# Optimization experiments

Measured on AMD Instinct MI355X. Metric: run time of the kernel, lower is better.

The kernel has to match this reference:

```python
import jax, jax.numpy as jnp
import numpy as np
import math

B, S, HID = 128, 200, 1024
NH = 4
DK = HID // NH
LSESS = 200  # session_len
MAXSEQ = 200
EPS = 1e-12


def setup_inputs() -> dict:
    key = jax.random.key(0)
    ks = jax.random.split(key, 12)
    inp = {}
    inp['query'] = jax.random.normal(ks[0], (B, S, HID), jnp.float32)
    inp['key'] = jax.random.normal(ks[1], (B, S, HID), jnp.float32)
    inp['value'] = jax.random.normal(ks[2], (B, S, HID), jnp.float32)
    std = 0.05
    inp['attn_w0'] = std * jax.random.normal(ks[3], (DK, DK), jnp.float32)
    inp['attn_w1'] = std * jax.random.normal(ks[4], (DK, DK), jnp.float32)
    inp['attn_w2'] = std * jax.random.normal(ks[5], (DK, DK), jnp.float32)
    inp['attn_w3'] = std * jax.random.normal(ks[6], (LSESS, DK), jnp.float32)
    inp['attn_bias'] = jnp.zeros((DK,), jnp.float32)
    inp['complex_weight'] = 0.02 * jax.random.normal(ks[7], (1, NH, MAXSEQ // 2 + 1, DK, 2), jnp.float32)
    bound = 1.0 / math.sqrt(HID)
    inp['linear_w'] = jax.random.uniform(ks[8], (HID, HID), jnp.float32, -bound, bound)
    inp['linear_b'] = jax.random.uniform(ks[9], (HID,), jnp.float32, -bound, bound)
    inp['ln_w'] = jnp.ones((HID,), jnp.float32)
    inp['ln_b'] = jnp.zeros((HID,), jnp.float32)
    return inp


def _gelu(x):
    return x * 0.5 * (1.0 + jax.lax.erf(x / jnp.sqrt(jnp.asarray(2.0, x.dtype))))


def reference(query, key, value, attn_w0, attn_w1, attn_w2, attn_w3, attn_bias,
              complex_weight, linear_w, linear_b, ln_w, ln_b):
    nb = query.shape[0]
    # (B, S, H, DK) -> (B, H, S, DK)
    def split_heads(x):
        return x.reshape(nb, -1, NH, DK).transpose(0, 2, 1, 3)
    q, k, v = split_heads(query), split_heads(key), split_heads(value)

    q = q @ attn_w0
    k = k @ attn_w1
    v = v @ attn_w2

    qf = jnp.fft.rfft(q, axis=2, norm='ortho')   # (B,H,S//2+1,DK) complex
    kf = jnp.fft.rfft(k, axis=2, norm='ortho')
    weight = complex_weight[..., 0] + 1j * complex_weight[..., 1]  # (1,4,MAXSEQ//2+1,DK)
    res = qf * jnp.conj(kf) * weight
    corr = jnp.fft.irfft(res, n=MAXSEQ, axis=2, norm='ortho')       # (B,H,MAXSEQ,DK)

    alpha = jnp.matmul(jax.nn.relu(corr + attn_bias), attn_w3.T)    # (B,H,MAXSEQ,LSESS)
    alpha = jax.nn.softmax(alpha, axis=-2)                          # softmax over seq dim
    x = jnp.einsum('bhsl,bhsd->bhld', alpha, v)                     # (B,H,LSESS,DK)

    x = x.transpose(0, 2, 1, 3).reshape(nb, -1, NH * DK)            # (B,LSESS,HID)
    x = x @ linear_w.T + linear_b
    # dropout is identity at inference
    x = _gelu(x)
    # LayerNorm (TF-style, eps inside sqrt)
    u = x.mean(-1, keepdims=True)
    s = ((x - u) ** 2).mean(-1, keepdims=True)
    x = (x - u) / jnp.sqrt(s + EPS)
    return ln_w * x + ln_b
```

## Files before the change

### kernel.cpp

```cpp
#include <hip/hip_runtime.h>
#include <hip/hip_bf16.h>
#include <math.h>

#define BATCH 128
#define SEQ   200
#define HID   1024
#define NH    4
#define DK    256
#define NF    101
#define NF2   202
#define LS    200
#define PD    256

typedef __attribute__((ext_vector_type(8))) short bf16x8;
typedef __attribute__((ext_vector_type(4))) float f32x4;

__device__ __forceinline__ unsigned short f2bf(float f) {
    union { float f; unsigned u; } v; v.f = f;
    unsigned r = v.u + 0x7fff + ((v.u >> 16) & 1);
    return (unsigned short)(r >> 16);
}
__device__ __forceinline__ float bf2f(unsigned short h) {
    union { unsigned u; float f; } v; v.u = ((unsigned)h) << 16;
    return v.f;
}

__device__ __forceinline__ void gld_lds16(const void* g, void* l) {
    __builtin_amdgcn_global_load_lds(
        (const __attribute__((address_space(1))) unsigned*)g,
        (__attribute__((address_space(3))) unsigned*)l, 16, 0, 0);
}

#define KSWZ(row, c8) ((c8) ^ (((row) & 7) << 3))

__global__ void init_tables_bf16(unsigned short* __restrict__ F, unsigned short* __restrict__ G) {
    int idx = blockIdx.x * 256 + threadIdx.x;
    const double inv = 0.07071067811865475244;
    const double PI2 = 6.283185307179586476925;
    {
        int fidx = idx >> 8, s = idx & 255;
        double v = 0.0;
        if (s < SEQ && fidx < NF2) {
            int f = (fidx < NF) ? fidx : fidx - NF;
            double ang = PI2 * (double)((f * s) % SEQ) / (double)SEQ;
            v = (fidx < NF) ? cos(ang) * inv : -sin(ang) * inv;
        }
        F[idx] = f2bf((float)v);
    }
    {
        int s = idx >> 8, j = idx & 255;
        double v = 0.0;
        if (s < SEQ && j < NF2) {
            if (j < NF) {
                double al = (j == 0 || j == NF - 1) ? 1.0 : 2.0;
                v = al * cos(PI2 * (double)((j * s) % SEQ) / (double)SEQ) * inv;
            } else {
                int f = j - NF;
                if (f != 0 && f != NF - 1)
                    v = -2.0 * sin(PI2 * (double)((f * s) % SEQ) / (double)SEQ) * inv;
            }
        }
        G[idx] = f2bf((float)v);
    }
}

__global__ void wtrans256(const float* __restrict__ src, unsigned short* __restrict__ dst) {
    int dout = blockIdx.x, din = threadIdx.x;
    dst[dout * 256 + din] = f2bf(src[din * 256 + dout]);
}

__global__ void w3pad(const float* __restrict__ src, unsigned short* __restrict__ dst) {
    int row = blockIdx.x, col = threadIdx.x;
    dst[row * 256 + col] = (row < LS) ? f2bf(src[row * 256 + col]) : (unsigned short)0;
}

__global__ void fconv(const float* __restrict__ src, unsigned short* __restrict__ dst, int n) {
    int i = blockIdx.x * 256 + threadIdx.x;
    if (i < n) dst[i] = f2bf(src[i]);
}

__global__ __launch_bounds__(256)
void mgemm128(const unsigned short* __restrict__ A, const float* __restrict__ Bf0,
              unsigned short* __restrict__ C0,
              int K, int lda, int ldb, int ldc,
              long aOuter, long aInner, long bOuter, long bInner,
              long cOuter, long cInner, int nInner, int nbValid) {
    int bz = blockIdx.z;
    int bo = bz / nInner, bi = bz - bo * nInner;
    const unsigned short* Ab = A + bo * aOuter + bi * aInner;
    const float* Bf = Bf0 + bo * bOuter + bi * bInner;

    __shared__ unsigned short As[128 * 64];
    __shared__ unsigned short Bs[128 * 64];

    int t = threadIdx.x;
    int m0 = blockIdx.y * 128, n0 = blockIdx.x * 128;
    int lane = t & 63, wave = t >> 6;
    int wr = wave >> 1, wc = wave & 1;
    int la = lane & 15, hi = lane >> 4;

    f32x4 acc[4][4] = {};
    int rsub = t >> 3;
    int c8 = (t & 7) * 8;

    for (int k0 = 0; k0 < K; k0 += 64) {
#pragma unroll
        for (int p = 0; p < 4; ++p) {
            int row = p * 32 + rsub;
            gld_lds16(Ab + (long)(m0 + row) * lda + k0 + KSWZ(row, c8), &As[row * 64 + c8]);
        }
#pragma unroll
        for (int p = 0; p < 4; ++p) {
            int row = p * 32 + rsub;
            int gn = n0 + row;
            unsigned short tmp[8];
            if (gn < nbValid) {
                const float4* src = reinterpret_cast<const float4*>(Bf + (long)gn * ldb + k0 + c8);
                float4 x0 = src[0], x1 = src[1];
                tmp[0] = f2bf(x0.x); tmp[1] = f2bf(x0.y); tmp[2] = f2bf(x0.z); tmp[3] = f2bf(x0.w);
                tmp[4] = f2bf(x1.x); tmp[5] = f2bf(x1.y); tmp[6] = f2bf(x1.z); tmp[7] = f2bf(x1.w);
            } else {
#pragma unroll
                for (int j = 0; j < 8; ++j) tmp[j] = 0;
            }
            *(bf16x8*)&Bs[row * 64 + KSWZ(row, c8)] = *(bf16x8*)tmp;
        }
        __syncthreads();
#pragma unroll
        for (int half = 0; half < 2; ++half) {
            int ko = half * 32 + hi * 8;
            bf16x8 a[4], b[4];
#pragma unroll
            for (int mi = 0; mi < 4; ++mi) {
                int ra = wr * 64 + mi * 16 + la;
                a[mi] = *(const bf16x8*)&As[ra * 64 + KSWZ(ra, ko)];
            }
#pragma unroll
            for (int ni = 0; ni < 4; ++ni) {
                int rb = wc * 64 + ni * 16 + la;
                b[ni] = *(const bf16x8*)&Bs[rb * 64 + KSWZ(rb, ko)];
            }
#pragma unroll
            for (int mi = 0; mi < 4; ++mi)
#pragma unroll
                for (int ni = 0; ni < 4; ++ni)
                    acc[mi][ni] = __builtin_amdgcn_mfma_f32_16x16x32_bf16(a[mi], b[ni], acc[mi][ni], 0, 0, 0);
        }
        __syncthreads();
    }

    unsigned short* Ch = C0 + bo * cOuter + bi * cInner;
#pragma unroll
    for (int mi = 0; mi < 4; ++mi) {
#pragma unroll
        for (int ni = 0; ni < 4; ++ni) {
            int gn = n0 + wc * 64 + ni * 16 + la;
            int gmB = m0 + wr * 64 + mi * 16 + hi * 4;
#pragma unroll
            for (int rr = 0; rr < 4; ++rr)
                Ch[(long)(gmB + rr) * ldc + gn] = f2bf(acc[mi][ni][rr]);
        }
    }
}

template <int EPI, bool XCDSWZ>
__global__ __launch_bounds__(512, 2)
void mgemm256(const unsigned short* __restrict__ A, const unsigned short* __restrict__ B,
              unsigned short* __restrict__ C0, int K, int lda, int ldb, int ldc,
              long aOuter, long aInner, long bOuter, long bInner,
              long cOuter, long cInner, int nInner, int mValid,
              const float* __restrict__ biasN) {
    extern __shared__ unsigned short lds[];
    unsigned short* AsB = lds;
    unsigned short* BsB = lds + 32768;

    int bx = blockIdx.x, by = blockIdx.y;
    if (XCDSWZ) {
        int nwg = gridDim.x * gridDim.y;
        int flat = by * gridDim.x + bx;
        int cpx = nwg >> 3;
        int swz = (flat & 7) * cpx + (flat >> 3);
        bx = swz % gridDim.x; by = swz / gridDim.x;
    }
    int bz = blockIdx.z;
    int bo = bz / nInner, bi = bz - bo * nInner;
    const unsigned short* Ab = A + bo * aOuter + bi * aInner;
    const unsigned short* Bb = B + bo * bOuter + bi * bInner;

    int t = threadIdx.x;
    int m0 = by * 256, n0 = bx * 256;
    int lane = t & 63, wave = t >> 6;
    int wr = wave >> 2, wc = wave & 3;
    int la = lane & 15, hi = lane >> 4;

    f32x4 acc[8][4] = {};
    int rsub = t >> 3;
    int c8 = (t & 7) * 8;

    auto stageA = [&](unsigned short* dst, long k0, int h) {
#pragma unroll
        for (int p = 0; p < 2; ++p) {
            int row = h * 128 + p * 64 + rsub;
            gld_lds16(Ab + (long)(m0 + row) * lda + k0 + KSWZ(row, c8), &dst[row * 64 + c8]);
        }
    };
    auto stageB = [&](unsigned short* dst, long k0, int h) {
#pragma unroll
        for (int p = 0; p < 2; ++p) {
            int row = h * 128 + p * 64 + rsub;
            gld_lds16(Bb + (long)(n0 + row) * ldb + k0 + KSWZ(row, c8), &dst[row * 64 + c8]);
        }
    };
    auto ldf = [&](const unsigned short* P, int row, int ko) -> bf16x8 {
        return *(const bf16x8*)&P[row * 64 + KSWZ(row, ko)];
    };

#define MFMA_ROW(mi, xa) \
    acc[mi][0] = __builtin_amdgcn_mfma_f32_16x16x32_bf16(xa, b0, acc[mi][0], 0, 0, 0); \
    acc[mi][1] = __builtin_amdgcn_mfma_f32_16x16x32_bf16(xa, b1, acc[mi][1], 0, 0, 0); \
    acc[mi][2] = __builtin_amdgcn_mfma_f32_16x16x32_bf16(xa, b2, acc[mi][2], 0, 0, 0); \
    acc[mi][3] = __builtin_amdgcn_mfma_f32_16x16x32_bf16(xa, b3, acc[mi][3], 0, 0, 0);

    int nkt = K >> 6;
    stageA(AsB, 0, 0); stageA(AsB, 0, 1);
    stageB(BsB, 0, 0); stageB(BsB, 0, 1);

    for (int kt = 0; kt < nkt; ++kt) {
        int cur = kt & 1;
        const unsigned short* Ac = AsB + cur * 16384;
        const unsigned short* Bc = BsB + cur * 16384;
        unsigned short* An = AsB + (cur ^ 1) * 16384;
        unsigned short* Bn = BsB + (cur ^ 1) * 16384;
        bool pre = (kt + 1) < nkt;
        long kn = (long)(kt + 1) << 6;

        bf16x8 b0, b1, b2, b3;

        if (pre) {
            stageA(An, kn, 0);
            asm volatile("s_waitcnt vmcnt(2)" ::: "memory");
        } else {
            asm volatile("s_waitcnt vmcnt(0)" ::: "memory");
        }
        __builtin_amdgcn_s_barrier();
        __builtin_amdgcn_sched_barrier(0);
        {
            int ko = hi * 8;
            b0 = ldf(Bc, wc * 64 + 0 * 16 + la, ko);
            b1 = ldf(Bc, wc * 64 + 1 * 16 + la, ko);
            b2 = ldf(Bc, wc * 64 + 2 * 16 + la, ko);
            b3 = ldf(Bc, wc * 64 + 3 * 16 + la, ko);
            bf16x8 x0 = ldf(Ac, wr * 128 + 0 * 16 + la, ko);
            bf16x8 x1 = ldf(Ac, wr * 128 + 1 * 16 + la, ko);
            bf16x8 x2 = ldf(Ac, wr * 128 + 2 * 16 + la, ko);
            bf16x8 x3 = ldf(Ac, wr * 128 + 3 * 16 + la, ko);
            __builtin_amdgcn_s_setprio(1);
            MFMA_ROW(0, x0) MFMA_ROW(1, x1) MFMA_ROW(2, x2) MFMA_ROW(3, x3)
            __builtin_amdgcn_s_setprio(0);
        }
        __builtin_amdgcn_s_barrier();

        if (pre) stageA(An, kn, 1);
        {
            int ko = hi * 8;
            bf16x8 x4 = ldf(Ac, wr * 128 + 4 * 16 + la, ko);
            bf16x8 x5 = ldf(Ac, wr * 128 + 5 * 16 + la, ko);
            bf16x8 x6 = ldf(Ac, wr * 128 + 6 * 16 + la, ko);
            bf16x8 x7 = ldf(Ac, wr * 128 + 7 * 16 + la, ko);
            __builtin_amdgcn_s_setprio(1);
            MFMA_ROW(4, x4) MFMA_ROW(5, x5) MFMA_ROW(6, x6) MFMA_ROW(7, x7)
            __builtin_amdgcn_s_setprio(0);
        }
        __builtin_amdgcn_s_barrier();

        if (pre) stageB(Bn, kn, 0);
        {
            int ko = 32 + hi * 8;
            b0 = ldf(Bc, wc * 64 + 0 * 16 + la, ko);
            b1 = ldf(Bc, wc * 64 + 1 * 16 + la, ko);
            b2 = ldf(Bc, wc * 64 + 2 * 16 + la, ko);
            b3 = ldf(Bc, wc * 64 + 3 * 16 + la, ko);
            bf16x8 x0 = ldf(Ac, wr * 128 + 0 * 16 + la, ko);
            bf16x8 x1 = ldf(Ac, wr * 128 + 1 * 16 + la, ko);
            bf16x8 x2 = ldf(Ac, wr * 128 + 2 * 16 + la, ko);
            bf16x8 x3 = ldf(Ac, wr * 128 + 3 * 16 + la, ko);
            __builtin_amdgcn_s_setprio(1);
            MFMA_ROW(0, x0) MFMA_ROW(1, x1) MFMA_ROW(2, x2) MFMA_ROW(3, x3)
            __builtin_amdgcn_s_setprio(0);
        }
        __builtin_amdgcn_s_barrier();

        if (pre) stageB(Bn, kn, 1);
        {
            int ko = 32 + hi * 8;
            bf16x8 x4 = ldf(Ac, wr * 128 + 4 * 16 + la, ko);
            bf16x8 x5 = ldf(Ac, wr * 128 + 5 * 16 + la, ko);
            bf16x8 x6 = ldf(Ac, wr * 128 + 6 * 16 + la, ko);
            bf16x8 x7 = ldf(Ac, wr * 128 + 7 * 16 + la, ko);
            __builtin_amdgcn_s_setprio(1);
            MFMA_ROW(4, x4) MFMA_ROW(5, x5) MFMA_ROW(6, x6) MFMA_ROW(7, x7)
            __builtin_amdgcn_s_setprio(0);
        }
        __builtin_amdgcn_s_barrier();
    }
#undef MFMA_ROW

    unsigned short* Ch = C0 + bo * cOuter + bi * cInner;
#pragma unroll
    for (int mi = 0; mi < 8; ++mi) {
#pragma unroll
        for (int ni = 0; ni < 4; ++ni) {
            int gn = n0 + wc * 64 + ni * 16 + la;
            int gmB = m0 + wr * 128 + mi * 16 + hi * 4;
            float bN = 0.f;
            if (EPI == 2 || EPI == 4) bN = biasN[gn];
#pragma unroll
            for (int rr = 0; rr < 4; ++rr) {
                int gm = gmB + rr;
                if (gm >= mValid) continue;
                float v = acc[mi][ni][rr];
                if (EPI == 0) Ch[(long)gm * ldc + gn] = f2bf(v);
                else if (EPI == 2) Ch[(long)gm * ldc + gn] = f2bf(fmaxf(v + bN, 0.f));
                else Ch[(long)gm * ldc + gn] = f2bf(v + bN);
            }
        }
    }
}

__global__ void crossspec(unsigned short* __restrict__ QF, const unsigned short* __restrict__ KF,
                          const float* __restrict__ cw) {
    long idx = (long)blockIdx.x * 256 + threadIdx.x;
    if (idx >= (long)BATCH * NH * DK * NF) return;
    int f = (int)(idx % NF);
    long tq = idx / NF;
    int d = (int)(tq % DK);
    int bh = (int)(tq / DK);
    int h = bh & (NH - 1);
    long base = (long)bh * DK * PD + (long)d * PD;
    float qr = bf2f(QF[base + f]), qi = bf2f(QF[base + NF + f]);
    float kr = bf2f(KF[base + f]), ki = bf2f(KF[base + NF + f]);
    float cr = qr * kr + qi * ki;
    float ci = qi * kr - qr * ki;
    long wb = (((long)h * NF + f) * DK + d) * 2;
    float wr = cw[wb], wi = cw[wb + 1];
    QF[base + f]      = f2bf(cr * wr - ci * wi);
    QF[base + NF + f] = f2bf(cr * wi + ci * wr);
    if (f < PD - NF2) QF[base + NF2 + f] = 0;
}

__global__ __launch_bounds__(256) void softmax_rows(const unsigned short* __restrict__ in,
                                                    unsigned short* __restrict__ out) {
    long row = (long)blockIdx.x * 4 + (threadIdx.x >> 6);
    int lane = threadIdx.x & 63;
    const unsigned short* p = in + row * PD;
    float v[4];
    float m = -1e30f;
#pragma unroll
    for (int i = 0; i < 4; ++i) {
        int s = lane + 64 * i;
        v[i] = (s < SEQ) ? bf2f(p[s]) : -1e30f;
        m = fmaxf(m, v[i]);
    }
#pragma unroll
    for (int o = 32; o; o >>= 1) m = fmaxf(m, __shfl_xor(m, o));
    float e[4], sum = 0.f;
#pragma unroll
    for (int i = 0; i < 4; ++i) {
        int s = lane + 64 * i;
        e[i] = (s < SEQ) ? expf(v[i] - m) : 0.f;
        sum += e[i];
    }
#pragma unroll
    for (int o = 32; o; o >>= 1) sum += __shfl_xor(sum, o);
    float inv = 1.f / sum;
    unsigned short* q = out + row * PD;
#pragma unroll
    for (int i = 0; i < 4; ++i) {
        int s = lane + 64 * i;
        q[s] = (s < SEQ) ? f2bf(e[i] * inv) : (unsigned short)0;
    }
}

__global__ __launch_bounds__(256) void gelu_ln_kernel(const unsigned short* __restrict__ y2,
                               const float* __restrict__ lnw, const float* __restrict__ lnb,
                               float* __restrict__ out) {
    long row = blockIdx.x;
    int tid = threadIdx.x;
    const short4* xr = reinterpret_cast<const short4*>(y2 + row * HID);
    short4 h4 = xr[tid];
    float g[4];
    {
        float x0 = bf2f((unsigned short)h4.x), x1 = bf2f((unsigned short)h4.y);
        float x2 = bf2f((unsigned short)h4.z), x3 = bf2f((unsigned short)h4.w);
        g[0] = 0.5f * x0 * (1.f + erff(x0 * 0.70710678118654752f));
        g[1] = 0.5f * x1 * (1.f + erff(x1 * 0.70710678118654752f));
        g[2] = 0.5f * x2 * (1.f + erff(x2 * 0.70710678118654752f));
        g[3] = 0.5f * x3 * (1.f + erff(x3 * 0.70710678118654752f));
    }

    __shared__ float red[4];
    float s = g[0] + g[1] + g[2] + g[3];
#pragma unroll
    for (int o = 32; o > 0; o >>= 1) s += __shfl_down(s, o);
    if ((tid & 63) == 0) red[tid >> 6] = s;
    __syncthreads();
    float mean = (red[0] + red[1] + red[2] + red[3]) * (1.f / (float)HID);

    float v2 = 0.f;
#pragma unroll
    for (int p = 0; p < 4; ++p) { float d = g[p] - mean; v2 += d * d; }
    __syncthreads();
#pragma unroll
    for (int o = 32; o > 0; o >>= 1) v2 += __shfl_down(v2, o);
    if ((tid & 63) == 0) red[tid >> 6] = v2;
    __syncthreads();
    float var = (red[0] + red[1] + red[2] + red[3]) * (1.f / (float)HID);
    float rstd = rsqrtf(var + 1e-12f);

    float4 o4;
    int i0 = tid * 4;
    o4.x = (g[0] - mean) * rstd * lnw[i0 + 0] + lnb[i0 + 0];
    o4.y = (g[1] - mean) * rstd * lnw[i0 + 1] + lnb[i0 + 1];
    o4.z = (g[2] - mean) * rstd * lnw[i0 + 2] + lnb[i0 + 2];
    o4.w = (g[3] - mean) * rstd * lnw[i0 + 3] + lnb[i0 + 3];
    reinterpret_cast<float4*>(out + row * HID)[tid] = o4;
}

extern "C" void kernel_launch(void* const* d_in, const int* in_sizes, int n_in,
                              void* d_out, int out_size, void* d_ws, size_t ws_size,
                              hipStream_t stream) {
    const float* query = (const float*)d_in[0];
    const float* key   = (const float*)d_in[1];
    const float* value = (const float*)d_in[2];
    const float* w0 = (const float*)d_in[3];
    const float* w1 = (const float*)d_in[4];
    const float* w2 = (const float*)d_in[5];
    const float* w3 = (const float*)d_in[6];
    const float* attn_bias = (const float*)d_in[7];
    const float* cw = (const float*)d_in[8];
    const float* lw = (const float*)d_in[9];
    const float* lb = (const float*)d_in[10];
    const float* lnw = (const float*)d_in[11];
    const float* lnb = (const float*)d_in[12];
    float* out = (float*)d_out;

    char* base = (char*)d_ws;
    const long BH = (long)BATCH * NH;
    const long SZR = (long)BH * PD * PD;
    const size_t M64 = 67108864;

    unsigned short* F_stack = (unsigned short*)(base + 0);
    unsigned short* G_stack = (unsigned short*)(base + 131072);
    unsigned short* w0T = (unsigned short*)(base + 262144);
    unsigned short* w1T = (unsigned short*)(base + 393216);
    unsigned short* w2T = (unsigned short*)(base + 524288);
    unsigned short* w3b = (unsigned short*)(base + 655360);
    unsigned short* lwb = (unsigned short*)(base + 786432);
    char* rA = base + 4194304;
    char* rB = rA + M64;
    char* rC = rB + M64;
    char* rD = rC + M64;
    char* rE = rD + M64;

    unsigned short* qpT = (unsigned short*)rA;
    unsigned short* kpT = (unsigned short*)rB;
    unsigned short* vpT = (unsigned short*)rC;
    unsigned short* QF  = (unsigned short*)rD;
    unsigned short* KF  = (unsigned short*)rE;
    unsigned short* corr = (unsigned short*)rA;
    unsigned short* alphaT = (unsigned short*)rD;
    unsigned short* probs = (unsigned short*)rB;
    unsigned short* X  = (unsigned short*)rE;
    unsigned short* y2 = (unsigned short*)rD;

    const size_t LDS256 = 131072;

    init_tables_bf16<<<256, 256, 0, stream>>>(F_stack, G_stack);
    wtrans256<<<256, 256, 0, stream>>>(w0, w0T);
    wtrans256<<<256, 256, 0, stream>>>(w1, w1T);
    wtrans256<<<256, 256, 0, stream>>>(w2, w2T);
    w3pad<<<256, 256, 0, stream>>>(w3, w3b);
    fconv<<<(HID * HID + 255) / 256, 256, 0, stream>>>(lw, lwb, HID * HID);

    dim3 gproj(2, 2, BH);
    mgemm128<<<gproj, 256, 0, stream>>>(w0T, query, qpT, DK, DK, HID, PD,
        0L, 0L, (long)SEQ * HID, (long)DK, (long)NH * PD * PD, (long)PD * PD, NH, SEQ);
    mgemm128<<<gproj, 256, 0, stream>>>(w1T, key, kpT, DK, DK, HID, PD,
        0L, 0L, (long)SEQ * HID, (long)DK, (long)NH * PD * PD, (long)PD * PD, NH, SEQ);
    mgemm128<<<gproj, 256, 0, stream>>>(w2T, value, vpT, DK, DK, HID, PD,
        0L, 0L, (long)SEQ * HID, (long)DK, (long)NH * PD * PD, (long)PD * PD, NH, SEQ);

    mgemm256<0, false><<<dim3(1, 1, 2 * BH), 512, LDS256, stream>>>(
        qpT, F_stack, QF, PD, PD, PD, PD,
        SZR, (long)PD * PD, 0L, 0L, SZR, (long)PD * PD, (int)BH, PD, nullptr);

    long ncs = (long)BH * DK * NF;
    crossspec<<<(unsigned)((ncs + 255) / 256), 256, 0, stream>>>(QF, KF, cw);

    mgemm256<2, false><<<dim3(1, 1, BH), 512, LDS256, stream>>>(
        G_stack, QF, corr, PD, PD, PD, PD,
        0L, 0L, (long)PD * PD, 0L, (long)PD * PD, 0L, 1, PD, attn_bias);

    mgemm256<0, false><<<dim3(1, 1, BH), 512, LDS256, stream>>>(
        w3b, corr, alphaT, PD, PD, PD, PD,
        0L, 0L, (long)PD * PD, 0L, (long)PD * PD, 0L, 1, PD, nullptr);

    softmax_rows<<<(unsigned)(BH * PD / 4), 256, 0, stream>>>(alphaT, probs);

    mgemm256<0, false><<<dim3(1, 1, BH), 512, LDS256, stream>>>(
        probs, vpT, X, PD, PD, PD, HID,
        (long)NH * PD * PD, (long)PD * PD,
        (long)NH * PD * PD, (long)PD * PD,
        (long)LS * HID, (long)DK, NH, LS, nullptr);

    mgemm256<4, true><<<dim3(HID / 256, (BATCH * LS) / 256, 1), 512, LDS256, stream>>>(
        X, lwb, y2, HID, HID, HID, HID,
        0L, 0L, 0L, 0L, 0L, 0L, 1, BATCH * LS, lb);

    gelu_ln_kernel<<<(unsigned)(BATCH * LS), 256, 0, stream>>>(y2, lnw, lnb, out);
}
```

Baseline: 605.1 us.

## Fuse alpha GEMM with softmax, merge QKV projections, vectorize cross-spectrum

The three QKV projection GEMMs are merged into one launch with 256x256 tiles, one block per (tensor, batch, head). The alpha GEMM and the separate softmax kernel become one kernel that does the softmax in registers using shuffles plus LDS reductions, so the alpha matrix never makes a round trip through global memory. The DFT tables now put the imaginary part at offset 128, which lets crossspec use aligned 8-wide vector loads with one block per batch-head. In exchange there is more register and LDS pressure in the fused kernel, and the projection kernel's B-operand staging is still synchronous.

```diff
diff --git a/kernel.cpp b/kernel.cpp
--- a/kernel.cpp
+++ b/kernel.cpp
@@ -8,9 +8,9 @@
 #define NH    4
 #define DK    256
 #define NF    101
-#define NF2   202
 #define LS    200
 #define PD    256
+#define IMOFF 128
 
 typedef __attribute__((ext_vector_type(8))) short bf16x8;
 typedef __attribute__((ext_vector_type(4))) float f32x4;
@@ -40,22 +40,25 @@
     {
         int fidx = idx >> 8, s = idx & 255;
         double v = 0.0;
-        if (s < SEQ && fidx < NF2) {
-            int f = (fidx < NF) ? fidx : fidx - NF;
-            double ang = PI2 * (double)((f * s) % SEQ) / (double)SEQ;
-            v = (fidx < NF) ? cos(ang) * inv : -sin(ang) * inv;
+        if (s < SEQ) {
+            if (fidx < NF) {
+                v = cos(PI2 * (double)((fidx * s) % SEQ) / (double)SEQ) * inv;
+            } else if (fidx >= IMOFF && fidx < IMOFF + NF) {
+                int f = fidx - IMOFF;
+                v = -sin(PI2 * (double)((f * s) % SEQ) / (double)SEQ) * inv;
+            }
         }
         F[idx] = f2bf((float)v);
     }
     {
         int s = idx >> 8, j = idx & 255;
         double v = 0.0;
-        if (s < SEQ && j < NF2) {
+        if (s < SEQ) {
             if (j < NF) {
                 double al = (j == 0 || j == NF - 1) ? 1.0 : 2.0;
                 v = al * cos(PI2 * (double)((j * s) % SEQ) / (double)SEQ) * inv;
-            } else {
-                int f = j - NF;
+            } else if (j >= IMOFF && j < IMOFF + NF) {
+                int f = j - IMOFF;
                 if (f != 0 && f != NF - 1)
                     v = -2.0 * sin(PI2 * (double)((f * s) % SEQ) / (double)SEQ) * inv;
             }
@@ -79,44 +82,43 @@
     if (i < n) dst[i] = f2bf(src[i]);
 }
 
-__global__ __launch_bounds__(256)
-void mgemm128(const unsigned short* __restrict__ A, const float* __restrict__ Bf0,
-              unsigned short* __restrict__ C0,
-              int K, int lda, int ldb, int ldc,
-              long aOuter, long aInner, long bOuter, long bInner,
-              long cOuter, long cInner, int nInner, int nbValid) {
-    int bz = blockIdx.z;
-    int bo = bz / nInner, bi = bz - bo * nInner;
-    const unsigned short* Ab = A + bo * aOuter + bi * aInner;
-    const float* Bf = Bf0 + bo * bOuter + bi * bInner;
-
-    __shared__ unsigned short As[128 * 64];
-    __shared__ unsigned short Bs[128 * 64];
+__global__ __launch_bounds__(512, 2)
+void mgemm256f(const unsigned short* __restrict__ Wall,
+               const float* __restrict__ Q, const float* __restrict__ Kt,
+               const float* __restrict__ V, unsigned short* __restrict__ C0) {
+    __shared__ unsigned short As[256 * 64];
+    __shared__ unsigned short Bs[256 * 64];
+
+    int bz = blockIdx.x;
+    int sel = bz >> 9;
+    int bh = bz & 511;
+    int b = bh >> 2, h = bh & 3;
+    const unsigned short* A = Wall + sel * 65536;
+    const float* Bf = ((sel == 0) ? Q : (sel == 1) ? Kt : V) + (long)b * SEQ * HID + h * DK;
+    unsigned short* Ch = C0 + (long)sel * 33554432 + (long)bh * PD * PD;
 
     int t = threadIdx.x;
-    int m0 = blockIdx.y * 128, n0 = blockIdx.x * 128;
     int lane = t & 63, wave = t >> 6;
-    int wr = wave >> 1, wc = wave & 1;
+    int wr = wave >> 2, wc = wave & 3;
     int la = lane & 15, hi = lane >> 4;
-
-    f32x4 acc[4][4] = {};
     int rsub = t >> 3;
     int c8 = (t & 7) * 8;
 
-    for (int k0 = 0; k0 < K; k0 += 64) {
+    f32x4 acc[8][4] = {};
+
+    for (int k0 = 0; k0 < 256; k0 += 64) {
 #pragma unroll
         for (int p = 0; p < 4; ++p) {
-            int row = p * 32 + rsub;
-            gld_lds16(Ab + (long)(m0 + row) * lda + k0 + KSWZ(row, c8), &As[row * 64 + c8]);
+            int row = p * 64 + rsub;
+            gld_lds16(A + (long)row * 256 + k0 + KSWZ(row, c8), &As[row * 64 + c8]);
         }
 #pragma unroll
         for (int p = 0; p < 4; ++p) {
-            int row = p * 32 + rsub;
-            int gn = n0 + row;
+            int row = p * 64 + rsub;
             unsigned short tmp[8];
-            if (gn < nbValid) {
-                const float4* src = reinterpret_cast<const float4*>(Bf + (long)gn * ldb + k0 + c8);
-                float4 x0 = src[0], x1 = src[1];
+            if (row < SEQ) {
+                const float4* s4 = reinterpret_cast<const float4*>(Bf + (long)row * HID + k0 + c8);
+                float4 x0 = s4[0], x1 = s4[1];
                 tmp[0] = f2bf(x0.x); tmp[1] = f2bf(x0.y); tmp[2] = f2bf(x0.z); tmp[3] = f2bf(x0.w);
                 tmp[4] = f2bf(x1.x); tmp[5] = f2bf(x1.y); tmp[6] = f2bf(x1.z); tmp[7] = f2bf(x1.w);
             } else {
@@ -129,36 +131,37 @@
 #pragma unroll
         for (int half = 0; half < 2; ++half) {
             int ko = half * 32 + hi * 8;
-            bf16x8 a[4], b[4];
-#pragma unroll
-            for (int mi = 0; mi < 4; ++mi) {
-                int ra = wr * 64 + mi * 16 + la;
-                a[mi] = *(const bf16x8*)&As[ra * 64 + KSWZ(ra, ko)];
-            }
+            bf16x8 bb[4], xx[8];
 #pragma unroll
             for (int ni = 0; ni < 4; ++ni) {
                 int rb = wc * 64 + ni * 16 + la;
-                b[ni] = *(const bf16x8*)&Bs[rb * 64 + KSWZ(rb, ko)];
-            }
-#pragma unroll
-            for (int mi = 0; mi < 4; ++mi)
+                bb[ni] = *(const bf16x8*)&Bs[rb * 64 + KSWZ(rb, ko)];
+            }
+#pragma unroll
+            for (int mi = 0; mi < 8; ++mi) {
+                int ra = wr * 128 + mi * 16 + la;
+                xx[mi] = *(const bf16x8*)&As[ra * 64 + KSWZ(ra, ko)];
+            }
+            __builtin_amdgcn_s_setprio(1);
+#pragma unroll
+            for (int mi = 0; mi < 8; ++mi)
 #pragma unroll
                 for (int ni = 0; ni < 4; ++ni)
-                    acc[mi][ni] = __builtin_amdgcn_mfma_f32_16x16x32_bf16(a[mi], b[ni], acc[mi][ni], 0, 0, 0);
+                    acc[mi][ni] = __builtin_amdgcn_mfma_f32_16x16x32_bf16(xx[mi], bb[ni], acc[mi][ni], 0, 0, 0);
+            __builtin_amdgcn_s_setprio(0);
         }
         __syncthreads();
     }
 
-    unsigned short* Ch = C0 + bo * cOuter + bi * cInner;
-#pragma unroll
-    for (int mi = 0; mi < 4; ++mi) {
+#pragma unroll
+    for (int mi = 0; mi < 8; ++mi) {
 #pragma unroll
         for (int ni = 0; ni < 4; ++ni) {
-            int gn = n0 + wc * 64 + ni * 16 + la;
-            int gmB = m0 + wr * 64 + mi * 16 + hi * 4;
+            int gn = wc * 64 + ni * 16 + la;
+            int gmB = wr * 128 + mi * 16 + hi * 4;
 #pragma unroll
             for (int rr = 0; rr < 4; ++rr)
-                Ch[(long)(gmB + rr) * ldc + gn] = f2bf(acc[mi][ni][rr]);
+                Ch[(long)(gmB + rr) * PD + gn] = f2bf(acc[mi][ni][rr]);
         }
     }
 }
@@ -327,57 +330,225 @@
     }
 }
 
-__global__ void crossspec(unsigned short* __restrict__ QF, const unsigned short* __restrict__ KF,
-                          const float* __restrict__ cw) {
-    long idx = (long)blockIdx.x * 256 + threadIdx.x;
-    if (idx >= (long)BATCH * NH * DK * NF) return;
-    int f = (int)(idx % NF);
-    long tq = idx / NF;
-    int d = (int)(tq % DK);
-    int bh = (int)(tq / DK);
+__global__ __launch_bounds__(512, 2)
+void alphasm(const unsigned short* __restrict__ A, const unsigned short* __restrict__ B,
+             unsigned short* __restrict__ P0) {
+    extern __shared__ unsigned short lds[];
+    unsigned short* AsB = lds;
+    unsigned short* BsB = lds + 32768;
+    __shared__ float redM[256][4];
+    __shared__ float redS[256][4];
+
+    int bh = blockIdx.x;
+    const unsigned short* Ab = A;
+    const unsigned short* Bb = B + (long)bh * PD * PD;
+
+    int t = threadIdx.x;
+    int lane = t & 63, wave = t >> 6;
+    int wr = wave >> 2, wc = wave & 3;
+    int la = lane & 15, hi = lane >> 4;
+
+    f32x4 acc[8][4] = {};
+    int rsub = t >> 3;
+    int c8 = (t & 7) * 8;
+
+    auto stageA = [&](unsigned short* dst, long k0, int h) {
+#pragma unroll
+        for (int p = 0; p < 2; ++p) {
+            int row = h * 128 + p * 64 + rsub;
+            gld_lds16(Ab + (long)row * PD + k0 + KSWZ(row, c8), &dst[row * 64 + c8]);
+        }
+    };
+    auto stageB = [&](unsigned short* dst, long k0, int h) {
+#pragma unroll
+        for (int p = 0; p < 2; ++p) {
+            int row = h * 128 + p * 64 + rsub;
+            gld_lds16(Bb + (long)row * PD + k0 + KSWZ(row, c8), &dst[row * 64 + c8]);
+        }
+    };
+    auto ldf = [&](const unsigned short* P, int row, int ko) -> bf16x8 {
+        return *(const bf16x8*)&P[row * 64 + KSWZ(row, ko)];
+    };
+
+#define MFMA_ROW(mi, xa) \
+    acc[mi][0] = __builtin_amdgcn_mfma_f32_16x16x32_bf16(xa, b0, acc[mi][0], 0, 0, 0); \
+    acc[mi][1] = __builtin_amdgcn_mfma_f32_16x16x32_bf16(xa, b1, acc[mi][1], 0, 0, 0); \
+    acc[mi][2] = __builtin_amdgcn_mfma_f32_16x16x32_bf16(xa, b2, acc[mi][2], 0, 0, 0); \
+    acc[mi][3] = __builtin_amdgcn_mfma_f32_16x16x32_bf16(xa, b3, acc[mi][3], 0, 0, 0);
+
+    stageA(AsB, 0, 0); stageA(AsB, 0, 1);
+    stageB(BsB, 0, 0); stageB(BsB, 0, 1);
+
+    for (int kt = 0; kt < 4; ++kt) {
+        int cur = kt & 1;
+        const unsigned short* Ac = AsB + cur * 16384;
+        const unsigned short* Bc = BsB + cur * 16384;
+        unsigned short* An = AsB + (cur ^ 1) * 16384;
+        unsigned short* Bn = BsB + (cur ^ 1) * 16384;
+        bool pre = kt < 3;
+        long kn = (long)(kt + 1) << 6;
+        bf16x8 b0, b1, b2, b3;
+
+        if (pre) {
+            stageA(An, kn, 0);
+            asm volatile("s_waitcnt vmcnt(2)" ::: "memory");
+        } else {
+            asm volatile("s_waitcnt vmcnt(0)" ::: "memory");
+        }
+        __builtin_amdgcn_s_barrier();
+        __builtin_amdgcn_sched_barrier(0);
+        {
+            int ko = hi * 8;
+            b0 = ldf(Bc, wc * 64 + 0 * 16 + la, ko);
+            b1 = ldf(Bc, wc * 64 + 1 * 16 + la, ko);
+            b2 = ldf(Bc, wc * 64 + 2 * 16 + la, ko);
+            b3 = ldf(Bc, wc * 64 + 3 * 16 + la, ko);
+            bf16x8 x0 = ldf(Ac, wr * 128 + 0 * 16 + la, ko);
+            bf16x8 x1 = ldf(Ac, wr * 128 + 1 * 16 + la, ko);
+            bf16x8 x2 = ldf(Ac, wr * 128 + 2 * 16 + la, ko);
+            bf16x8 x3 = ldf(Ac, wr * 128 + 3 * 16 + la, ko);
+            __builtin_amdgcn_s_setprio(1);
+            MFMA_ROW(0, x0) MFMA_ROW(1, x1) MFMA_ROW(2, x2) MFMA_ROW(3, x3)
+            __builtin_amdgcn_s_setprio(0);
+        }
+        __builtin_amdgcn_s_barrier();
+        if (pre) stageA(An, kn, 1);
+        {
+            int ko = hi * 8;
+            bf16x8 x4 = ldf(Ac, wr * 128 + 4 * 16 + la, ko);
+            bf16x8 x5 = ldf(Ac, wr * 128 + 5 * 16 + la, ko);
+            bf16x8 x6 = ldf(Ac, wr * 128 + 6 * 16 + la, ko);
+            bf16x8 x7 = ldf(Ac, wr * 128 + 7 * 16 + la, ko);
+            __builtin_amdgcn_s_setprio(1);
+            MFMA_ROW(4, x4) MFMA_ROW(5, x5) MFMA_ROW(6, x6) MFMA_ROW(7, x7)
+            __builtin_amdgcn_s_setprio(0);
+        }
+        __builtin_amdgcn_s_barrier();
+        if (pre) stageB(Bn, kn, 0);
+        {
+            int ko = 32 + hi * 8;
+            b0 = ldf(Bc, wc * 64 + 0 * 16 + la, ko);
+            b1 = ldf(Bc, wc * 64 + 1 * 16 + la, ko);
+            b2 = ldf(Bc, wc * 64 + 2 * 16 + la, ko);
+            b3 = ldf(Bc, wc * 64 + 3 * 16 + la, ko);
+            bf16x8 x0 = ldf(Ac, wr * 128 + 0 * 16 + la, ko);
+            bf16x8 x1 = ldf(Ac, wr * 128 + 1 * 16 + la, ko);
+            bf16x8 x2 = ldf(Ac, wr * 128 + 2 * 16 + la, ko);
+            bf16x8 x3 = ldf(Ac, wr * 128 + 3 * 16 + la, ko);
+            __builtin_amdgcn_s_setprio(1);
+            MFMA_ROW(0, x0) MFMA_ROW(1, x1) MFMA_ROW(2, x2) MFMA_ROW(3, x3)
+            __builtin_amdgcn_s_setprio(0);
+        }
+        __builtin_amdgcn_s_barrier();
+        if (pre) stageB(Bn, kn, 1);
+        {
+            int ko = 32 + hi * 8;
+            bf16x8 x4 = ldf(Ac, wr * 128 + 4 * 16 + la, ko);
+            bf16x8 x5 = ldf(Ac, wr * 128 + 5 * 16 + la, ko);
+            bf16x8 x6 = ldf(Ac, wr * 128 + 6 * 16 + la, ko);
+            bf16x8 x7 = ldf(Ac, wr * 128 + 7 * 16 + la, ko);
+            __builtin_amdgcn_s_setprio(1);
+            MFMA_ROW(4, x4) MFMA_ROW(5, x5) MFMA_ROW(6, x6) MFMA_ROW(7, x7)
+            __builtin_amdgcn_s_setprio(0);
+        }
+        __builtin_amdgcn_s_barrier();
+    }
+#undef MFMA_ROW
+
+#pragma unroll
+    for (int mi = 0; mi < 8; ++mi) {
+#pragma unroll
+        for (int rr = 0; rr < 4; ++rr) {
+            float mv = -1e30f;
+#pragma unroll
+            for (int ni = 0; ni < 4; ++ni) {
+                int gn = wc * 64 + ni * 16 + la;
+                if (gn < LS) mv = fmaxf(mv, acc[mi][ni][rr]);
+            }
+            mv = fmaxf(mv, __shfl_xor(mv, 1));
+            mv = fmaxf(mv, __shfl_xor(mv, 2));
+            mv = fmaxf(mv, __shfl_xor(mv, 4));
+            mv = fmaxf(mv, __shfl_xor(mv, 8));
+            if (la == 0) redM[wr * 128 + mi * 16 + hi * 4 + rr][wc] = mv;
+        }
+    }
+    __syncthreads();
+#pragma unroll
+    for (int mi = 0; mi < 8; ++mi) {
+#pragma unroll
+        for (int rr = 0; rr < 4; ++rr) {
+            int row = wr * 128 + mi * 16 + hi * 4 + rr;
+            float m = fmaxf(fmaxf(redM[row][0], redM[row][1]),
+                            fmaxf(redM[row][2], redM[row][3]));
+            float s = 0.f;
+#pragma unroll
+            for (int ni = 0; ni < 4; ++ni) {
+                int gn = wc * 64 + ni * 16 + la;
+                float e = (gn < LS) ? __expf(acc[mi][ni][rr] - m) : 0.f;
+                acc[mi][ni][rr] = e;
+                s += e;
+            }
+            s += __shfl_xor(s, 1);
+            s += __shfl_xor(s, 2);
+            s += __shfl_xor(s, 4);
+            s += __shfl_xor(s, 8);
+            if (la == 0) redS[row][wc] = s;
+        }
+    }
+    __syncthreads();
+    unsigned short* P = lds;
+#pragma unroll
+    for (int mi = 0; mi < 8; ++mi) {
+#pragma unroll
+        for (int rr = 0; rr < 4; ++rr) {
+            int row = wr * 128 + mi * 16 + hi * 4 + rr;
+            float inv = 1.f / (redS[row][0] + redS[row][1] + redS[row][2] + redS[row][3]);
+#pragma unroll
+            for (int ni = 0; ni < 4; ++ni) {
+                int gn = wc * 64 + ni * 16 + la;
+                P[row * 256 + gn] = f2bf(acc[mi][ni][rr] * inv);
+            }
+        }
+    }
+    __syncthreads();
+    unsigned short* Pg = P0 + (long)bh * PD * PD;
+    for (int i = t; i < 256 * 32; i += 512) {
+        int row = i >> 5, seg = (i & 31) * 8;
+        *(bf16x8*)(Pg + (long)row * PD + seg) = *(const bf16x8*)&P[row * 256 + seg];
+    }
+}
+
+__global__ __launch_bounds__(256)
+void crossspec(unsigned short* __restrict__ QF, const unsigned short* __restrict__ KF,
+               const float* __restrict__ cw) {
+    int bh = blockIdx.x;
     int h = bh & (NH - 1);
-    long base = (long)bh * DK * PD + (long)d * PD;
-    float qr = bf2f(QF[base + f]), qi = bf2f(QF[base + NF + f]);
-    float kr = bf2f(KF[base + f]), ki = bf2f(KF[base + NF + f]);
-    float cr = qr * kr + qi * ki;
-    float ci = qi * kr - qr * ki;
-    long wb = (((long)h * NF + f) * DK + d) * 2;
-    float wr = cw[wb], wi = cw[wb + 1];
-    QF[base + f]      = f2bf(cr * wr - ci * wi);
-    QF[base + NF + f] = f2bf(cr * wi + ci * wr);
-    if (f < PD - NF2) QF[base + NF2 + f] = 0;
-}
-
-__global__ __launch_bounds__(256) void softmax_rows(const unsigned short* __restrict__ in,
-                                                    unsigned short* __restrict__ out) {
-    long row = (long)blockIdx.x * 4 + (threadIdx.x >> 6);
-    int lane = threadIdx.x & 63;
-    const unsigned short* p = in + row * PD;
-    float v[4];
-    float m = -1e30f;
-#pragma unroll
-    for (int i = 0; i < 4; ++i) {
-        int s = lane + 64 * i;
-        v[i] = (s < SEQ) ? bf2f(p[s]) : -1e30f;
-        m = fmaxf(m, v[i]);
-    }
-#pragma unroll
-    for (int o = 32; o; o >>= 1) m = fmaxf(m, __shfl_xor(m, o));
-    float e[4], sum = 0.f;
-#pragma unroll
-    for (int i = 0; i < 4; ++i) {
-        int s = lane + 64 * i;
-        e[i] = (s < SEQ) ? expf(v[i] - m) : 0.f;
-        sum += e[i];
-    }
-#pragma unroll
-    for (int o = 32; o; o >>= 1) sum += __shfl_xor(sum, o);
-    float inv = 1.f / sum;
-    unsigned short* q = out + row * PD;
-#pragma unroll
-    for (int i = 0; i < 4; ++i) {
-        int s = lane + 64 * i;
-        q[s] = (s < SEQ) ? f2bf(e[i] * inv) : (unsigned short)0;
+    long qbase = (long)bh * DK * PD;
+    for (int i = threadIdx.x; i < DK * 13; i += 256) {
+        int d = i / 13, fg = i - d * 13;
+        long rb = qbase + (long)d * PD + fg * 8;
+        bf16x8 qre = *(const bf16x8*)(QF + rb);
+        bf16x8 qim = *(const bf16x8*)(QF + rb + IMOFF);
+        bf16x8 kre = *(const bf16x8*)(KF + rb);
+        bf16x8 kim = *(const bf16x8*)(KF + rb + IMOFF);
+        bf16x8 orr, oii;
+#pragma unroll
+        for (int j = 0; j < 8; ++j) {
+            int f = fg * 8 + j;
+            float qr = bf2f((unsigned short)qre[j]), qi = bf2f((unsigned short)qim[j]);
+            float kr = bf2f((unsigned short)kre[j]), ki = bf2f((unsigned short)kim[j]);
+            float cr = qr * kr + qi * ki;
+            float ci = qi * kr - qr * ki;
+            float wr = 0.f, wi = 0.f;
+            if (f < NF) {
+                long wb = (((long)h * NF + f) * DK + d) * 2;
+                wr = cw[wb]; wi = cw[wb + 1];
+            }
+            orr[j] = (short)f2bf(cr * wr - ci * wi);
+            oii[j] = (short)f2bf(cr * wi + ci * wr);
+        }
+        *(bf16x8*)(QF + rb) = orr;
+        *(bf16x8*)(QF + rb + IMOFF) = oii;
     }
 }
 
@@ -452,8 +623,6 @@
     unsigned short* F_stack = (unsigned short*)(base + 0);
     unsigned short* G_stack = (unsigned short*)(base + 131072);
     unsigned short* w0T = (unsigned short*)(base + 262144);
-    unsigned short* w1T = (unsigned short*)(base + 393216);
-    unsigned short* w2T = (unsigned short*)(base + 524288);
     unsigned short* w3b = (unsigned short*)(base + 655360);
     unsigned short* lwb = (unsigned short*)(base + 786432);
     char* rA = base + 4194304;
@@ -468,7 +637,6 @@
     unsigned short* QF  = (unsigned short*)rD;
     unsigned short* KF  = (unsigned short*)rE;
     unsigned short* corr = (unsigned short*)rA;
-    unsigned short* alphaT = (unsigned short*)rD;
     unsigned short* probs = (unsigned short*)rB;
     unsigned short* X  = (unsigned short*)rE;
     unsigned short* y2 = (unsigned short*)rD;
@@ -477,35 +645,24 @@
 
     init_tables_bf16<<<256, 256, 0, stream>>>(F_stack, G_stack);
     wtrans256<<<256, 256, 0, stream>>>(w0, w0T);
-    wtrans256<<<256, 256, 0, stream>>>(w1, w1T);
-    wtrans256<<<256, 256, 0, stream>>>(w2, w2T);
+    wtrans256<<<256, 256, 0, stream>>>(w1, w0T + 65536);
+    wtrans256<<<256, 256, 0, stream>>>(w2, w0T + 131072);
     w3pad<<<256, 256, 0, stream>>>(w3, w3b);
     fconv<<<(HID * HID + 255) / 256, 256, 0, stream>>>(lw, lwb, HID * HID);
 
-    dim3 gproj(2, 2, BH);
-    mgemm128<<<gproj, 256, 0, stream>>>(w0T, query, qpT, DK, DK, HID, PD,
-        0L, 0L, (long)SEQ * HID, (long)DK, (long)NH * PD * PD, (long)PD * PD, NH, SEQ);
-    mgemm128<<<gproj, 256, 0, stream>>>(w1T, key, kpT, DK, DK, HID, PD,
-        0L, 0L, (long)SEQ * HID, (long)DK, (long)NH * PD * PD, (long)PD * PD, NH, SEQ);
-    mgemm128<<<gproj, 256, 0, stream>>>(w2T, value, vpT, DK, DK, HID, PD,
-        0L, 0L, (long)SEQ * HID, (long)DK, (long)NH * PD * PD, (long)PD * PD, NH, SEQ);
+    mgemm256f<<<dim3(3 * 512, 1, 1), 512, 0, stream>>>(w0T, query, key, value, qpT);
 
     mgemm256<0, false><<<dim3(1, 1, 2 * BH), 512, LDS256, stream>>>(
         qpT, F_stack, QF, PD, PD, PD, PD,
         SZR, (long)PD * PD, 0L, 0L, SZR, (long)PD * PD, (int)BH, PD, nullptr);
 
-    long ncs = (long)BH * DK * NF;
-    crossspec<<<(unsigned)((ncs + 255) / 256), 256, 0, stream>>>(QF, KF, cw);
+    crossspec<<<(unsigned)BH, 256, 0, stream>>>(QF, KF, cw);
 
     mgemm256<2, false><<<dim3(1, 1, BH), 512, LDS256, stream>>>(
         G_stack, QF, corr, PD, PD, PD, PD,
         0L, 0L, (long)PD * PD, 0L, (long)PD * PD, 0L, 1, PD, attn_bias);
 
-    mgemm256<0, false><<<dim3(1, 1, BH), 512, LDS256, stream>>>(
-        w3b, corr, alphaT, PD, PD, PD, PD,
-        0L, 0L, (long)PD * PD, 0L, (long)PD * PD, 0L, 1, PD, nullptr);
-
-    softmax_rows<<<(unsigned)(BH * PD / 4), 256, 0, stream>>>(alphaT, probs);
+    alphasm<<<dim3((unsigned)BH, 1, 1), 512, LDS256, stream>>>(w3b, corr, probs);
 
     mgemm256<0, false><<<dim3(1, 1, BH), 512, LDS256, stream>>>(
         probs, vpT, X, PD, PD, PD, HID,
```

Measured after the change: 613.8 us. Within noise of the previous version (+1.4%).
